# Kernel tuning notes

Hardware: AMD Instinct MI355X
Metric: run time of the kernel (lower is better)

The kernel has to match this reference:

```python
import jax, jax.numpy as jnp
import numpy as np

FORGET_BIAS = 1.0  # TF BasicLSTMCell default


def _lstm_scan(xs, kernel, bias):
    """xs: [T, B, D]; kernel: [D+H, 4H]; bias: [4H]. Returns hs: [T, B, H]."""
    hidden = bias.shape[0] // 4
    batch = xs.shape[1]

    def step(carry, x):
        c, h = carry
        z = jnp.concatenate([x, h], axis=-1) @ kernel + bias
        i, j, f, o = jnp.split(z, 4, axis=-1)  # TF gate order: input, candidate, forget, output
        c_new = c * jax.nn.sigmoid(f + FORGET_BIAS) + jax.nn.sigmoid(i) * jnp.tanh(j)
        h_new = jnp.tanh(c_new) * jax.nn.sigmoid(o)
        return (c_new, h_new), h_new

    init = (jnp.zeros((batch, hidden), xs.dtype), jnp.zeros((batch, hidden), xs.dtype))
    _, hs = jax.lax.scan(step, init, xs)
    return hs


def setup_inputs() -> dict:
    key = jax.random.key(0)
    ks = jax.random.split(key, 8)
    B, T, D, H, V, L = 128, 512, 128, 128, 50000, 19
    return {
        "input_ids": jax.random.randint(ks[0], (B, T), 0, V, dtype=jnp.int32),
        "embedding_table": jax.random.normal(ks[1], (V, D), jnp.float32) * 0.02,
        "fw_kernel": jax.random.normal(ks[2], (D + H, 4 * H), jnp.float32) * 0.05,
        "fw_bias": jnp.zeros((4 * H,), jnp.float32),
        "bw_kernel": jax.random.normal(ks[3], (D + H, 4 * H), jnp.float32) * 0.05,
        "bw_bias": jnp.zeros((4 * H,), jnp.float32),
        "att_w": jax.random.normal(ks[4], (H,), jnp.float32) * 0.1,
        "fc_w": jax.random.normal(ks[5], (H, L), jnp.float32) * 0.1,
        "fc_b": jnp.zeros((L,), jnp.float32),
    }


def reference(input_ids, embedding_table, fw_kernel, fw_bias, bw_kernel, bw_bias, att_w, fc_w, fc_b):
    # Embedding lookup: [B, T, D]
    x = embedding_table[input_ids]
    xs = jnp.transpose(x, (1, 0, 2))  # [T, B, D] time-major for scan

    fw = jnp.transpose(_lstm_scan(xs, fw_kernel, fw_bias), (1, 0, 2))           # [B, T, H]
    bw = jnp.transpose(_lstm_scan(xs[::-1], bw_kernel, bw_bias)[::-1], (1, 0, 2))  # [B, T, H]

    Hsum = fw + bw                         # [B, T, H]
    M = jnp.tanh(Hsum)
    scores = jnp.einsum('bth,h->bt', M, att_w)
    alpha = jax.nn.softmax(scores, axis=-1)            # [B, T]
    r = jnp.einsum('bth,bt->bh', Hsum, alpha)          # attention-pooled [B, H]
    h_star = jnp.tanh(r)                               # keep_prob=1.0 -> dropout is identity

    logits = h_star @ fc_w + fc_b                      # [B, L]
    probabilities = jnp.argmax(jax.nn.softmax(logits, axis=-1), axis=1)
    predict_label_ids = jnp.argmax(logits, axis=1)
    l2_loss = 0.5 * (jnp.sum(fc_w * fc_w) + jnp.sum(fc_b * fc_b))  # tf.nn.l2_loss
    return logits, predict_label_ids, l2_loss, probabilities
```

## Files before the change

kernel.cpp:

```cpp
#include <hip/hip_runtime.h>

typedef unsigned short u16;
typedef unsigned int u32;
typedef short short8 __attribute__((ext_vector_type(8)));
typedef float f32x4 __attribute__((ext_vector_type(4)));

#define T_LEN 512
#define NCLS 19

#define L2E 1.4426950408889634f
#define TL2E 2.8853901617765067f

static __device__ __forceinline__ u16 f2bf(float f) {
  u32 u = __float_as_uint(f);
  u32 r = (u + 0x7FFFu + ((u >> 16) & 1u)) >> 16;
  return (u16)r;
}
static __device__ __forceinline__ float bf2f(u16 h) {
  return __uint_as_float(((u32)h) << 16);
}
static __device__ __forceinline__ float rcp_f(float x) { return __builtin_amdgcn_rcpf(x); }
static __device__ __forceinline__ float ex2(float x) { return __builtin_amdgcn_exp2f(x); }

__global__ __launch_bounds__(256) void k_embed(const int* __restrict__ ids,
                                               const float* __restrict__ table,
                                               u16* __restrict__ xs) {
  int i = blockIdx.x * 256 + threadIdx.x;
  int e = i * 4;
  int m = e >> 7;
  int col = e & 127;
  int t = m >> 7, b = m & 127;
  int id = ids[b * T_LEN + t];
  float4 v = *(const float4*)(table + (size_t)id * 128 + col);
  ushort4 o;
  o.x = f2bf(v.x); o.y = f2bf(v.y); o.z = f2bf(v.z); o.w = f2bf(v.w);
  *(ushort4*)(xs + (size_t)m * 128 + col) = o;
}

__global__ __launch_bounds__(256) void k_prep(const float* __restrict__ fw_k,
                                              const float* __restrict__ bw_k,
                                              const float* __restrict__ fw_b,
                                              const float* __restrict__ bw_b,
                                              u16* __restrict__ wt_bf,
                                              float* __restrict__ bias_pre) {
  int wg = blockIdx.x;
  int tid = threadIdx.x;
  if (wg < 1024) {
    int i = wg * 256 + tid;
    int n = i >> 8, k = i & 255;
    int dir = n >> 9, p = n & 511;
    int w = p >> 6, nt = (p >> 4) & 3, g4 = (p >> 2) & 3, q = p & 3;
    int u = w * 16 + g4 * 4 + nt;
    int j = q * 128 + u;
    float sc = (q == 1) ? TL2E : L2E;
    const float* K = dir ? bw_k : fw_k;
    wt_bf[i] = f2bf(K[k * 512 + j] * sc);
  } else {
    for (int uu = 0; uu < 4; uu++) {
      int n = uu * 256 + tid;
      int dir = n >> 9, p = n & 511;
      int w = p >> 6, nt = (p >> 4) & 3, g4 = (p >> 2) & 3, q = p & 3;
      int u = w * 16 + g4 * 4 + nt;
      int j = q * 128 + u;
      float sc = (q == 1) ? TL2E : L2E;
      float bv = (dir ? bw_b : fw_b)[j] + (q == 2 ? 1.0f : 0.0f);
      bias_pre[n] = bv * sc;
    }
  }
}

__global__ __launch_bounds__(512, 2) void k_lstm(const u16* __restrict__ wt_bf,
                                                 const float* __restrict__ bias_pre,
                                                 const u16* __restrict__ xs,
                                                 u16* __restrict__ hs_fw,
                                                 u16* __restrict__ hs_bw) {
  __shared__ u16 hbuf[2][4][144];
  __shared__ float xstage[16][524];
  int tid = threadIdx.x;
  int wg = blockIdx.x;
  int dir = wg >> 5;
  int bb = (wg & 31) * 4;
  int w = tid >> 6, l = tid & 63;
  int cb = l & 15, g4 = l >> 4;
  int cbv = cb & 3;
  int so = cb >> 2;

  short8 wf[32];
#pragma unroll
  for (int n = 0; n < 4; n++) {
    const u16* wb = wt_bf + ((size_t)(dir * 512 + w * 64 + n * 16 + cb) * 256) + g4 * 8;
#pragma unroll
    for (int ks = 0; ks < 8; ks++)
      wf[n * 8 + ks] = *(const short8*)(wb + ks * 32);
  }
  f32x4 bias4[4];
#pragma unroll
  for (int n = 0; n < 4; n++)
    bias4[n] = *(const f32x4*)(bias_pre + dir * 512 + w * 64 + n * 16 + g4 * 4);

  float c = 0.0f;
  int u_so = w * 16 + g4 * 4 + so;

  int roff[4];
#pragma unroll
  for (int ks = 0; ks < 4; ks++)
    roff[ks] = cbv * 288 + ks * 64 + g4 * 16;
  int xcol = w * 256 + g4 * 16;

  u32* hz = (u32*)hbuf;
  hz[tid >= 512 ? 0 : tid] = 0;
  if (tid < 64) hz[512 + tid] = 0;
  __syncthreads();

  int t0a = dir ? (T_LEN - 1) : 0;
  int stp = dir ? -1 : 1;
  u16* hsout = dir ? hs_bw : hs_fw;
  long step1 = (long)stp * 16384;

  const u16* xb0 = xs + ((size_t)(t0a * 128 + bb + cbv) * 128) + g4 * 8;
  u16* ph = hsout + ((size_t)(t0a * 128 + bb + cbv) * 128) + u_so;

  short8 xblk[4];
  {
    const u16* p = xb0 + (long)so * step1;
#pragma unroll
    for (int ks = 0; ks < 4; ks++) xblk[ks] = *(const short8*)(p + ks * 32);
  }
#pragma unroll
  for (int n = 0; n < 4; n++) {
    f32x4 xacc = bias4[n];
    xacc = __builtin_amdgcn_mfma_f32_16x16x32_bf16(wf[n * 8 + 0], xblk[0], xacc, 0, 0, 0);
    xacc = __builtin_amdgcn_mfma_f32_16x16x32_bf16(wf[n * 8 + 1], xblk[1], xacc, 0, 0, 0);
    xacc = __builtin_amdgcn_mfma_f32_16x16x32_bf16(wf[n * 8 + 2], xblk[2], xacc, 0, 0, 0);
    xacc = __builtin_amdgcn_mfma_f32_16x16x32_bf16(wf[n * 8 + 3], xblk[3], xacc, 0, 0, 0);
    *(f32x4*)((char*)&xstage[cb][0] + xcol + n * 64) = xacc;
  }
  {
    const u16* p = xb0 + (long)(4 + so) * step1;
#pragma unroll
    for (int ks = 0; ks < 4; ks++) xblk[ks] = *(const short8*)(p + ks * 32);
  }
  asm volatile("s_waitcnt lgkmcnt(0)" ::: "memory");
  __builtin_amdgcn_s_barrier();
  asm volatile("" ::: "memory");

  for (int t = 0; t < T_LEN; t++) {
    int CUR = t & 1, NXT = CUR ^ 1;
    const char* hrow = (const char*)&hbuf[CUR][0][0];
    short8 hf0 = *(const short8*)(hrow + roff[0]);
    short8 hf1 = *(const short8*)(hrow + roff[1]);
    short8 hf2 = *(const short8*)(hrow + roff[2]);
    short8 hf3 = *(const short8*)(hrow + roff[3]);
    f32x4 a0 = {0.f, 0.f, 0.f, 0.f}, a1 = a0, a2 = a0, a3 = a0;
    a0 = __builtin_amdgcn_mfma_f32_16x16x32_bf16(wf[4],  hf0, a0, 0, 0, 0);
    a1 = __builtin_amdgcn_mfma_f32_16x16x32_bf16(wf[12], hf0, a1, 0, 0, 0);
    a2 = __builtin_amdgcn_mfma_f32_16x16x32_bf16(wf[20], hf0, a2, 0, 0, 0);
    a3 = __builtin_amdgcn_mfma_f32_16x16x32_bf16(wf[28], hf0, a3, 0, 0, 0);
    a0 = __builtin_amdgcn_mfma_f32_16x16x32_bf16(wf[5],  hf1, a0, 0, 0, 0);
    a1 = __builtin_amdgcn_mfma_f32_16x16x32_bf16(wf[13], hf1, a1, 0, 0, 0);
    a2 = __builtin_amdgcn_mfma_f32_16x16x32_bf16(wf[21], hf1, a2, 0, 0, 0);
    a3 = __builtin_amdgcn_mfma_f32_16x16x32_bf16(wf[29], hf1, a3, 0, 0, 0);
    a0 = __builtin_amdgcn_mfma_f32_16x16x32_bf16(wf[6],  hf2, a0, 0, 0, 0);
    a1 = __builtin_amdgcn_mfma_f32_16x16x32_bf16(wf[14], hf2, a1, 0, 0, 0);
    a2 = __builtin_amdgcn_mfma_f32_16x16x32_bf16(wf[22], hf2, a2, 0, 0, 0);
    a3 = __builtin_amdgcn_mfma_f32_16x16x32_bf16(wf[30], hf2, a3, 0, 0, 0);
    a0 = __builtin_amdgcn_mfma_f32_16x16x32_bf16(wf[7],  hf3, a0, 0, 0, 0);
    a1 = __builtin_amdgcn_mfma_f32_16x16x32_bf16(wf[15], hf3, a1, 0, 0, 0);
    a2 = __builtin_amdgcn_mfma_f32_16x16x32_bf16(wf[23], hf3, a2, 0, 0, 0);
    a3 = __builtin_amdgcn_mfma_f32_16x16x32_bf16(wf[31], hf3, a3, 0, 0, 0);
    f32x4 zA = (so & 2) ? a2 : a0;
    f32x4 zB = (so & 2) ? a3 : a1;
    f32x4 zh = (so & 1) ? zB : zA;
    f32x4 zx = *(const f32x4*)&xstage[(t & 3) * 4 + cbv][w * 64 + so * 16 + g4 * 4];
    float z0 = zh[0] + zx[0];
    float z1 = zh[1] + zx[1];
    float z2 = zh[2] + zx[2];
    float z3 = zh[3] + zx[3];
    float A2 = ex2(-z0);
    float B2 = ex2(z1);
    float F2 = ex2(-z2);
    float O2 = ex2(-z3);
    float r1 = rcp_f((1.f + A2) * (1.f + B2));
    float rf = rcp_f(1.f + F2);
    float cn = fmaf(c, rf, (B2 - 1.f) * r1);
    c = cn;
    float C2 = ex2(cn * TL2E);
    float r2 = rcp_f((1.f + C2) * (1.f + O2));
    float hv = (C2 - 1.f) * r2;
    u16 hb16 = f2bf(hv);
    hbuf[NXT][cbv][u_so] = hb16;
    *ph = hb16;
    ph += step1;
    asm volatile("s_waitcnt lgkmcnt(0)" ::: "memory");
    __builtin_amdgcn_s_barrier();
    asm volatile("" ::: "memory");
    if ((t & 3) == 3 && t < 508) {
#pragma unroll
      for (int n = 0; n < 4; n++) {
        f32x4 xacc = bias4[n];
        xacc = __builtin_amdgcn_mfma_f32_16x16x32_bf16(wf[n * 8 + 0], xblk[0], xacc, 0, 0, 0);
        xacc = __builtin_amdgcn_mfma_f32_16x16x32_bf16(wf[n * 8 + 1], xblk[1], xacc, 0, 0, 0);
        xacc = __builtin_amdgcn_mfma_f32_16x16x32_bf16(wf[n * 8 + 2], xblk[2], xacc, 0, 0, 0);
        xacc = __builtin_amdgcn_mfma_f32_16x16x32_bf16(wf[n * 8 + 3], xblk[3], xacc, 0, 0, 0);
        *(f32x4*)((char*)&xstage[cb][0] + xcol + n * 64) = xacc;
      }
      int ts = t + 5 + so;
      if (ts > 511) ts = 511;
      const u16* p = xb0 + (long)ts * step1;
#pragma unroll
      for (int ks = 0; ks < 4; ks++) xblk[ks] = *(const short8*)(p + ks * 32);
      asm volatile("s_waitcnt lgkmcnt(0)" ::: "memory");
      __builtin_amdgcn_s_barrier();
      asm volatile("" ::: "memory");
    }
  }
}

__global__ __launch_bounds__(512) void k_attn(const u16* __restrict__ hsf,
                                              const u16* __restrict__ hsb,
                                              const float* __restrict__ att_w,
                                              const float* __restrict__ fc_w,
                                              const float* __restrict__ fc_b,
                                              float* __restrict__ out) {
  __shared__ float rsum[8][128];
  __shared__ float esums[8];
  __shared__ float hstar[128];
  __shared__ float lg[NCLS];
  int tid = threadIdx.x, b = blockIdx.x;
  int w = tid >> 6, l = tid & 63;
  float2 aw = *(const float2*)(att_w + 2 * l);
  float r0 = 0.f, r1 = 0.f, es = 0.f;
  for (int t = w; t < T_LEN; t += 8) {
    size_t o = ((size_t)t * 128 + b) * 128 + 2 * l;
    u32 vf = *(const u32*)(hsf + o);
    u32 vb = *(const u32*)(hsb + o);
    float h0 = bf2f((u16)vf) + bf2f((u16)vb);
    float h1 = bf2f((u16)(vf >> 16)) + bf2f((u16)(vb >> 16));
    float e0 = ex2(h0 * TL2E);
    float th0 = (e0 - 1.f) * rcp_f(e0 + 1.f);
    float e1 = ex2(h1 * TL2E);
    float th1 = (e1 - 1.f) * rcp_f(e1 + 1.f);
    float s = fmaf(th0, aw.x, th1 * aw.y);
#pragma unroll
    for (int o2 = 32; o2 >= 1; o2 >>= 1) s += __shfl_xor(s, o2, 64);
    float e = ex2(s * L2E);
    r0 = fmaf(e, h0, r0); r1 = fmaf(e, h1, r1); es += e;
  }
  rsum[w][2 * l] = r0;
  rsum[w][2 * l + 1] = r1;
  if (l == 0) esums[w] = es;
  __syncthreads();
  if (tid < 128) {
    float r = 0.f, et = 0.f;
#pragma unroll
    for (int i = 0; i < 8; i++) { r += rsum[i][tid]; et += esums[i]; }
    float rr = r / et;
    float e2 = ex2(rr * TL2E);
    hstar[tid] = (e2 - 1.f) * rcp_f(e2 + 1.f);
  }
  __syncthreads();
  if (tid < NCLS) {
    float acc = fc_b[tid];
#pragma unroll 4
    for (int hh = 0; hh < 128; hh++) acc = fmaf(hstar[hh], fc_w[hh * NCLS + tid], acc);
    out[b * NCLS + tid] = acc;
    lg[tid] = acc;
  }
  __syncthreads();
  if (tid == 0) {
    int best = 0; float bv = lg[0];
    for (int l2 = 1; l2 < NCLS; l2++)
      if (lg[l2] > bv) { bv = lg[l2]; best = l2; }
    out[2432 + b] = (float)best;
    out[2561 + b] = (float)best;
  }
}

__global__ __launch_bounds__(256) void k_l2(const float* __restrict__ fc_w,
                                            const float* __restrict__ fc_b,
                                            float* __restrict__ out) {
  __shared__ float red[256];
  int tid = threadIdx.x;
  float a = 0.f;
  for (int i = tid; i < 128 * NCLS; i += 256) a += fc_w[i] * fc_w[i];
  if (tid < NCLS) a += fc_b[tid] * fc_b[tid];
  red[tid] = a; __syncthreads();
  for (int s = 128; s >= 1; s >>= 1) {
    if (tid < s) red[tid] += red[tid + s];
    __syncthreads();
  }
  if (tid == 0) out[2560] = 0.5f * red[0];
}

extern "C" void kernel_launch(void* const* d_in, const int* in_sizes, int n_in,
                              void* d_out, int out_size, void* d_ws, size_t ws_size,
                              hipStream_t stream) {
  const int* ids = (const int*)d_in[0];
  const float* table = (const float*)d_in[1];
  const float* fw_k = (const float*)d_in[2];
  const float* fw_b = (const float*)d_in[3];
  const float* bw_k = (const float*)d_in[4];
  const float* bw_b = (const float*)d_in[5];
  const float* att_w = (const float*)d_in[6];
  const float* fc_w = (const float*)d_in[7];
  const float* fc_b = (const float*)d_in[8];
  float* out = (float*)d_out;
  char* ws = (char*)d_ws;

  u16* xs = (u16*)(ws + 0);
  u16* wt_bf = (u16*)(ws + 16777216);
  float* bias_pre = (float*)(ws + 17301504);
  u16* hs_fw = (u16*)(ws + 17305600);
  u16* hs_bw = (u16*)(ws + 34082816);

  hipLaunchKernelGGL(k_embed, dim3(8192), dim3(256), 0, stream, ids, table, xs);
  hipLaunchKernelGGL(k_prep, dim3(1025), dim3(256), 0, stream, fw_k, bw_k, fw_b, bw_b,
                     wt_bf, bias_pre);
  hipLaunchKernelGGL(k_lstm, dim3(64), dim3(512), 0, stream, wt_bf, bias_pre, xs,
                     hs_fw, hs_bw);
  hipLaunchKernelGGL(k_attn, dim3(128), dim3(512), 0, stream, hs_fw, hs_bw, att_w,
                     fc_w, fc_b, out);
  hipLaunchKernelGGL(k_l2, dim3(1), dim3(256), 0, stream, fc_w, fc_b, out);
}
```

Before: 356.5 us.

## Double-buffer x-projection stage to drop extra barrier and merge small kernels

The LSTM recurrence now double-buffers the precomputed input-projection staging area in shared memory. Each block of four timesteps writes the next block's projection into the alternate buffer, which removes the second barrier that previously guarded xstage reuse every fourth step. The embedding and weight-prep kernels are merged into one launch, and the L2-loss kernel becomes an extra block of the attention kernel, cutting two launches. The cost is more shared memory in the LSTM kernel, which may limit its 2-blocks-per-CU occupancy target.

```diff
diff --git a/kernel.cpp b/kernel.cpp
--- a/kernel.cpp
+++ b/kernel.cpp
@@ -22,31 +22,30 @@
 static __device__ __forceinline__ float rcp_f(float x) { return __builtin_amdgcn_rcpf(x); }
 static __device__ __forceinline__ float ex2(float x) { return __builtin_amdgcn_exp2f(x); }
 
-__global__ __launch_bounds__(256) void k_embed(const int* __restrict__ ids,
-                                               const float* __restrict__ table,
-                                               u16* __restrict__ xs) {
-  int i = blockIdx.x * 256 + threadIdx.x;
-  int e = i * 4;
-  int m = e >> 7;
-  int col = e & 127;
-  int t = m >> 7, b = m & 127;
-  int id = ids[b * T_LEN + t];
-  float4 v = *(const float4*)(table + (size_t)id * 128 + col);
-  ushort4 o;
-  o.x = f2bf(v.x); o.y = f2bf(v.y); o.z = f2bf(v.z); o.w = f2bf(v.w);
-  *(ushort4*)(xs + (size_t)m * 128 + col) = o;
-}
-
-__global__ __launch_bounds__(256) void k_prep(const float* __restrict__ fw_k,
-                                              const float* __restrict__ bw_k,
-                                              const float* __restrict__ fw_b,
-                                              const float* __restrict__ bw_b,
-                                              u16* __restrict__ wt_bf,
-                                              float* __restrict__ bias_pre) {
+__global__ __launch_bounds__(256) void k_embed_prep(const int* __restrict__ ids,
+                                                    const float* __restrict__ table,
+                                                    const float* __restrict__ fw_k,
+                                                    const float* __restrict__ bw_k,
+                                                    const float* __restrict__ fw_b,
+                                                    const float* __restrict__ bw_b,
+                                                    u16* __restrict__ xs,
+                                                    u16* __restrict__ wt_bf,
+                                                    float* __restrict__ bias_pre) {
   int wg = blockIdx.x;
   int tid = threadIdx.x;
-  if (wg < 1024) {
+  if (wg < 8192) {
     int i = wg * 256 + tid;
+    int e = i * 4;
+    int m = e >> 7;
+    int col = e & 127;
+    int t = m >> 7, b = m & 127;
+    int id = ids[b * T_LEN + t];
+    float4 v = *(const float4*)(table + (size_t)id * 128 + col);
+    ushort4 o;
+    o.x = f2bf(v.x); o.y = f2bf(v.y); o.z = f2bf(v.z); o.w = f2bf(v.w);
+    *(ushort4*)(xs + (size_t)m * 128 + col) = o;
+  } else if (wg < 9216) {
+    int i = (wg - 8192) * 256 + tid;
     int n = i >> 8, k = i & 255;
     int dir = n >> 9, p = n & 511;
     int w = p >> 6, nt = (p >> 4) & 3, g4 = (p >> 2) & 3, q = p & 3;
@@ -75,7 +74,7 @@
                                                  u16* __restrict__ hs_fw,
                                                  u16* __restrict__ hs_bw) {
   __shared__ u16 hbuf[2][4][144];
-  __shared__ float xstage[16][524];
+  __shared__ float xstage[2][16][524];
   int tid = threadIdx.x;
   int wg = blockIdx.x;
   int dir = wg >> 5;
@@ -133,7 +132,7 @@
     xacc = __builtin_amdgcn_mfma_f32_16x16x32_bf16(wf[n * 8 + 1], xblk[1], xacc, 0, 0, 0);
     xacc = __builtin_amdgcn_mfma_f32_16x16x32_bf16(wf[n * 8 + 2], xblk[2], xacc, 0, 0, 0);
     xacc = __builtin_amdgcn_mfma_f32_16x16x32_bf16(wf[n * 8 + 3], xblk[3], xacc, 0, 0, 0);
-    *(f32x4*)((char*)&xstage[cb][0] + xcol + n * 64) = xacc;
+    *(f32x4*)((char*)&xstage[0][cb][0] + xcol + n * 64) = xacc;
   }
   {
     const u16* p = xb0 + (long)(4 + so) * step1;
@@ -144,71 +143,71 @@
   __builtin_amdgcn_s_barrier();
   asm volatile("" ::: "memory");
 
-  for (int t = 0; t < T_LEN; t++) {
-    int CUR = t & 1, NXT = CUR ^ 1;
-    const char* hrow = (const char*)&hbuf[CUR][0][0];
-    short8 hf0 = *(const short8*)(hrow + roff[0]);
-    short8 hf1 = *(const short8*)(hrow + roff[1]);
-    short8 hf2 = *(const short8*)(hrow + roff[2]);
-    short8 hf3 = *(const short8*)(hrow + roff[3]);
-    f32x4 a0 = {0.f, 0.f, 0.f, 0.f}, a1 = a0, a2 = a0, a3 = a0;
-    a0 = __builtin_amdgcn_mfma_f32_16x16x32_bf16(wf[4],  hf0, a0, 0, 0, 0);
-    a1 = __builtin_amdgcn_mfma_f32_16x16x32_bf16(wf[12], hf0, a1, 0, 0, 0);
-    a2 = __builtin_amdgcn_mfma_f32_16x16x32_bf16(wf[20], hf0, a2, 0, 0, 0);
-    a3 = __builtin_amdgcn_mfma_f32_16x16x32_bf16(wf[28], hf0, a3, 0, 0, 0);
-    a0 = __builtin_amdgcn_mfma_f32_16x16x32_bf16(wf[5],  hf1, a0, 0, 0, 0);
-    a1 = __builtin_amdgcn_mfma_f32_16x16x32_bf16(wf[13], hf1, a1, 0, 0, 0);
-    a2 = __builtin_amdgcn_mfma_f32_16x16x32_bf16(wf[21], hf1, a2, 0, 0, 0);
-    a3 = __builtin_amdgcn_mfma_f32_16x16x32_bf16(wf[29], hf1, a3, 0, 0, 0);
-    a0 = __builtin_amdgcn_mfma_f32_16x16x32_bf16(wf[6],  hf2, a0, 0, 0, 0);
-    a1 = __builtin_amdgcn_mfma_f32_16x16x32_bf16(wf[14], hf2, a1, 0, 0, 0);
-    a2 = __builtin_amdgcn_mfma_f32_16x16x32_bf16(wf[22], hf2, a2, 0, 0, 0);
-    a3 = __builtin_amdgcn_mfma_f32_16x16x32_bf16(wf[30], hf2, a3, 0, 0, 0);
-    a0 = __builtin_amdgcn_mfma_f32_16x16x32_bf16(wf[7],  hf3, a0, 0, 0, 0);
-    a1 = __builtin_amdgcn_mfma_f32_16x16x32_bf16(wf[15], hf3, a1, 0, 0, 0);
-    a2 = __builtin_amdgcn_mfma_f32_16x16x32_bf16(wf[23], hf3, a2, 0, 0, 0);
-    a3 = __builtin_amdgcn_mfma_f32_16x16x32_bf16(wf[31], hf3, a3, 0, 0, 0);
-    f32x4 zA = (so & 2) ? a2 : a0;
-    f32x4 zB = (so & 2) ? a3 : a1;
-    f32x4 zh = (so & 1) ? zB : zA;
-    f32x4 zx = *(const f32x4*)&xstage[(t & 3) * 4 + cbv][w * 64 + so * 16 + g4 * 4];
-    float z0 = zh[0] + zx[0];
-    float z1 = zh[1] + zx[1];
-    float z2 = zh[2] + zx[2];
-    float z3 = zh[3] + zx[3];
-    float A2 = ex2(-z0);
-    float B2 = ex2(z1);
-    float F2 = ex2(-z2);
-    float O2 = ex2(-z3);
-    float r1 = rcp_f((1.f + A2) * (1.f + B2));
-    float rf = rcp_f(1.f + F2);
-    float cn = fmaf(c, rf, (B2 - 1.f) * r1);
-    c = cn;
-    float C2 = ex2(cn * TL2E);
-    float r2 = rcp_f((1.f + C2) * (1.f + O2));
-    float hv = (C2 - 1.f) * r2;
-    u16 hb16 = f2bf(hv);
-    hbuf[NXT][cbv][u_so] = hb16;
-    *ph = hb16;
-    ph += step1;
-    asm volatile("s_waitcnt lgkmcnt(0)" ::: "memory");
-    __builtin_amdgcn_s_barrier();
-    asm volatile("" ::: "memory");
-    if ((t & 3) == 3 && t < 508) {
-#pragma unroll
-      for (int n = 0; n < 4; n++) {
-        f32x4 xacc = bias4[n];
-        xacc = __builtin_amdgcn_mfma_f32_16x16x32_bf16(wf[n * 8 + 0], xblk[0], xacc, 0, 0, 0);
-        xacc = __builtin_amdgcn_mfma_f32_16x16x32_bf16(wf[n * 8 + 1], xblk[1], xacc, 0, 0, 0);
-        xacc = __builtin_amdgcn_mfma_f32_16x16x32_bf16(wf[n * 8 + 2], xblk[2], xacc, 0, 0, 0);
-        xacc = __builtin_amdgcn_mfma_f32_16x16x32_bf16(wf[n * 8 + 3], xblk[3], xacc, 0, 0, 0);
-        *(f32x4*)((char*)&xstage[cb][0] + xcol + n * 64) = xacc;
+  for (int tt = 0; tt < 128; tt++) {
+    int bs = tt & 1;
+#pragma unroll
+    for (int j = 0; j < 4; j++) {
+      const char* hrow = (const char*)&hbuf[j & 1][0][0];
+      short8 hf0 = *(const short8*)(hrow + roff[0]);
+      short8 hf1 = *(const short8*)(hrow + roff[1]);
+      short8 hf2 = *(const short8*)(hrow + roff[2]);
+      short8 hf3 = *(const short8*)(hrow + roff[3]);
+      f32x4 a0 = {0.f, 0.f, 0.f, 0.f}, a1 = a0, a2 = a0, a3 = a0;
+      a0 = __builtin_amdgcn_mfma_f32_16x16x32_bf16(wf[4],  hf0, a0, 0, 0, 0);
+      a1 = __builtin_amdgcn_mfma_f32_16x16x32_bf16(wf[12], hf0, a1, 0, 0, 0);
+      a2 = __builtin_amdgcn_mfma_f32_16x16x32_bf16(wf[20], hf0, a2, 0, 0, 0);
+      a3 = __builtin_amdgcn_mfma_f32_16x16x32_bf16(wf[28], hf0, a3, 0, 0, 0);
+      a0 = __builtin_amdgcn_mfma_f32_16x16x32_bf16(wf[5],  hf1, a0, 0, 0, 0);
+      a1 = __builtin_amdgcn_mfma_f32_16x16x32_bf16(wf[13], hf1, a1, 0, 0, 0);
+      a2 = __builtin_amdgcn_mfma_f32_16x16x32_bf16(wf[21], hf1, a2, 0, 0, 0);
+      a3 = __builtin_amdgcn_mfma_f32_16x16x32_bf16(wf[29], hf1, a3, 0, 0, 0);
+      a0 = __builtin_amdgcn_mfma_f32_16x16x32_bf16(wf[6],  hf2, a0, 0, 0, 0);
+      a1 = __builtin_amdgcn_mfma_f32_16x16x32_bf16(wf[14], hf2, a1, 0, 0, 0);
+      a2 = __builtin_amdgcn_mfma_f32_16x16x32_bf16(wf[22], hf2, a2, 0, 0, 0);
+      a3 = __builtin_amdgcn_mfma_f32_16x16x32_bf16(wf[30], hf2, a3, 0, 0, 0);
+      a0 = __builtin_amdgcn_mfma_f32_16x16x32_bf16(wf[7],  hf3, a0, 0, 0, 0);
+      a1 = __builtin_amdgcn_mfma_f32_16x16x32_bf16(wf[15], hf3, a1, 0, 0, 0);
+      a2 = __builtin_amdgcn_mfma_f32_16x16x32_bf16(wf[23], hf3, a2, 0, 0, 0);
+      a3 = __builtin_amdgcn_mfma_f32_16x16x32_bf16(wf[31], hf3, a3, 0, 0, 0);
+      f32x4 zA = (so & 2) ? a2 : a0;
+      f32x4 zB = (so & 2) ? a3 : a1;
+      f32x4 zh = (so & 1) ? zB : zA;
+      f32x4 zx = *(const f32x4*)&xstage[bs][j * 4 + cbv][w * 64 + so * 16 + g4 * 4];
+      float z0 = zh[0] + zx[0];
+      float z1 = zh[1] + zx[1];
+      float z2 = zh[2] + zx[2];
+      float z3 = zh[3] + zx[3];
+      float A2 = ex2(-z0);
+      float B2 = ex2(z1);
+      float F2 = ex2(-z2);
+      float O2 = ex2(-z3);
+      float r1 = rcp_f((1.f + A2) * (1.f + B2));
+      float rf = rcp_f(1.f + F2);
+      float cn = fmaf(c, rf, (B2 - 1.f) * r1);
+      c = cn;
+      float C2 = ex2(cn * TL2E);
+      float r2 = rcp_f((1.f + C2) * (1.f + O2));
+      float hv = (C2 - 1.f) * r2;
+      u16 hb16 = f2bf(hv);
+      hbuf[(j & 1) ^ 1][cbv][u_so] = hb16;
+      *ph = hb16;
+      ph += step1;
+      if (j == 3 && tt < 127) {
+#pragma unroll
+        for (int n = 0; n < 4; n++) {
+          f32x4 xacc = bias4[n];
+          xacc = __builtin_amdgcn_mfma_f32_16x16x32_bf16(wf[n * 8 + 0], xblk[0], xacc, 0, 0, 0);
+          xacc = __builtin_amdgcn_mfma_f32_16x16x32_bf16(wf[n * 8 + 1], xblk[1], xacc, 0, 0, 0);
+          xacc = __builtin_amdgcn_mfma_f32_16x16x32_bf16(wf[n * 8 + 2], xblk[2], xacc, 0, 0, 0);
+          xacc = __builtin_amdgcn_mfma_f32_16x16x32_bf16(wf[n * 8 + 3], xblk[3], xacc, 0, 0, 0);
+          *(f32x4*)((char*)&xstage[bs ^ 1][cb][0] + xcol + n * 64) = xacc;
+        }
+        int ts = 4 * tt + 8 + so;
+        if (ts > 511) ts = 511;
+        const u16* p = xb0 + (long)ts * step1;
+#pragma unroll
+        for (int ks = 0; ks < 4; ks++) xblk[ks] = *(const short8*)(p + ks * 32);
       }
-      int ts = t + 5 + so;
-      if (ts > 511) ts = 511;
-      const u16* p = xb0 + (long)ts * step1;
-#pragma unroll
-      for (int ks = 0; ks < 4; ks++) xblk[ks] = *(const short8*)(p + ks * 32);
       asm volatile("s_waitcnt lgkmcnt(0)" ::: "memory");
       __builtin_amdgcn_s_barrier();
       asm volatile("" ::: "memory");
@@ -228,6 +227,22 @@
   __shared__ float lg[NCLS];
   int tid = threadIdx.x, b = blockIdx.x;
   int w = tid >> 6, l = tid & 63;
+  if (b == 128) {
+    float a = 0.f;
+    for (int i = tid; i < 128 * NCLS; i += 512) a += fc_w[i] * fc_w[i];
+    if (tid < NCLS) a += fc_b[tid] * fc_b[tid];
+#pragma unroll
+    for (int o2 = 32; o2 >= 1; o2 >>= 1) a += __shfl_xor(a, o2, 64);
+    if (l == 0) esums[w] = a;
+    __syncthreads();
+    if (tid == 0) {
+      float s = 0.f;
+#pragma unroll
+      for (int i = 0; i < 8; i++) s += esums[i];
+      out[2560] = 0.5f * s;
+    }
+    return;
+  }
   float2 aw = *(const float2*)(att_w + 2 * l);
   float r0 = 0.f, r1 = 0.f, es = 0.f;
   for (int t = w; t < T_LEN; t += 8) {
@@ -274,22 +289,6 @@
     out[2432 + b] = (float)best;
     out[2561 + b] = (float)best;
   }
-}
-
-__global__ __launch_bounds__(256) void k_l2(const float* __restrict__ fc_w,
-                                            const float* __restrict__ fc_b,
-                                            float* __restrict__ out) {
-  __shared__ float red[256];
-  int tid = threadIdx.x;
-  float a = 0.f;
-  for (int i = tid; i < 128 * NCLS; i += 256) a += fc_w[i] * fc_w[i];
-  if (tid < NCLS) a += fc_b[tid] * fc_b[tid];
-  red[tid] = a; __syncthreads();
-  for (int s = 128; s >= 1; s >>= 1) {
-    if (tid < s) red[tid] += red[tid + s];
-    __syncthreads();
-  }
-  if (tid == 0) out[2560] = 0.5f * red[0];
 }
 
 extern "C" void kernel_launch(void* const* d_in, const int* in_sizes, int n_in,
@@ -313,12 +312,10 @@
   u16* hs_fw = (u16*)(ws + 17305600);
   u16* hs_bw = (u16*)(ws + 34082816);
 
-  hipLaunchKernelGGL(k_embed, dim3(8192), dim3(256), 0, stream, ids, table, xs);
-  hipLaunchKernelGGL(k_prep, dim3(1025), dim3(256), 0, stream, fw_k, bw_k, fw_b, bw_b,
-                     wt_bf, bias_pre);
+  hipLaunchKernelGGL(k_embed_prep, dim3(9217), dim3(256), 0, stream, ids, table,
+                     fw_k, bw_k, fw_b, bw_b, xs, wt_bf, bias_pre);
   hipLaunchKernelGGL(k_lstm, dim3(64), dim3(512), 0, stream, wt_bf, bias_pre, xs,
                      hs_fw, hs_bw);
-  hipLaunchKernelGGL(k_attn, dim3(128), dim3(512), 0, stream, hs_fw, hs_bw, att_w,
+  hipLaunchKernelGGL(k_attn, dim3(129), dim3(512), 0, stream, hs_fw, hs_bw, att_w,
                      fc_w, fc_b, out);
-  hipLaunchKernelGGL(k_l2, dim3(1), dim3(256), 0, stream, fc_w, fc_b, out);
-}
+}
```

Result: slower. 373.6 us (+4.8%).
